# Optimization experiments

Hardware: AMD Instinct MI355X
Metric: run time of the kernel (lower is better)

## Reference

```python
import jax, jax.numpy as jnp
import numpy as np

VOCAB = 50000
SEQ = 2048
BATCH = 64
D = 256


def setup_inputs() -> dict:
    key = jax.random.key(0)
    ks = jax.random.split(key, 9)
    x = jax.random.randint(ks[0], (SEQ, BATCH), 0, VOCAB)  # token ids, 0 = pad
    emb = jax.random.normal(ks[1], (VOCAB, D), jnp.float32) * 0.02
    emb = emb.at[0].set(0.0)  # padding_idx=0
    idf = jax.random.uniform(ks[2], (VOCAB,), jnp.float32, 0.1, 10.0)
    W1 = jax.random.normal(ks[3], (100, D), jnp.float32) * (1.0 / np.sqrt(D))
    b1 = jax.random.normal(ks[4], (100,), jnp.float32) * 0.01
    W2 = jax.random.normal(ks[5], (150, 100), jnp.float32) * 0.1
    b2 = jax.random.normal(ks[6], (150,), jnp.float32) * 0.01
    W3 = jax.random.normal(ks[7], (2, 150), jnp.float32) * 0.1
    b3 = jax.random.normal(ks[8], (2,), jnp.float32) * 0.01
    return {"x": x, "emb": emb, "idf": idf, "W1": W1, "b1": b1,
            "W2": W2, "b2": b2, "W3": W3, "b3": b3}


def reference(x, emb, idf, W1, b1, W2, b2, W3, b3):
    tokens = x.T  # [B, S] (nums = x.permute(1, 0))
    vocab = emb.shape[0]

    # per-row term frequency: histogram (scatter-add) then gather back
    def tf_row(row):  # row: [S] int
        return jnp.zeros((vocab,), jnp.float32).at[row].add(1.0)[row]

    tf = jax.vmap(tf_row)(tokens)                      # [B, S]
    scores = jnp.where(tokens == 0, 0.0, tf * idf[tokens])  # [B, S]

    # bmm of (B, D, S) with (B, S, 1) == tf-idf weighted sum of embeddings
    pooled = jnp.einsum('bsd,bs->bd', emb[tokens], scores)  # [B, D]

    h = jax.nn.relu(pooled @ W1.T + b1)
    h = jax.nn.relu(h @ W2.T + b2)
    return jax.nn.softmax(h @ W3.T + b3, axis=-1)  # [B, 2]
```

## Files before the change

kernel.cpp:

```cpp
#include <hip/hip_runtime.h>

#define VOCAB 50000
#define SEQ   2048
#define BATCH 64
#define DIM   256
#define NC    16
#define CHUNK (SEQ / NC)
#define H1    100
#define H2    150
#define HASH  4096

__global__ __launch_bounds__(1024)
void k_scores(const int* __restrict__ x,
              const float* __restrict__ idf,
              float* __restrict__ scores) {
    __shared__ int   tok[SEQ];
    __shared__ int   hkey[HASH];
    __shared__ int   hcnt[HASH];
    const int b = blockIdx.x;
    const int t = threadIdx.x;

    for (int i = t; i < HASH; i += 1024) { hkey[i] = -1; hcnt[i] = 0; }
    for (int s = t; s < SEQ; s += 1024)  tok[s] = x[s * BATCH + b];
    __syncthreads();

    for (int s = t; s < SEQ; s += 1024) {
        const int mytok = tok[s];
        unsigned h = ((unsigned)mytok * 2654435761u) >> 20;
        while (true) {
            int prev = atomicCAS(&hkey[h], -1, mytok);
            if (prev == -1 || prev == mytok) { atomicAdd(&hcnt[h], 1); break; }
            h = (h + 1) & (HASH - 1);
        }
    }
    __syncthreads();

    for (int s = t; s < SEQ; s += 1024) {
        const int mytok = tok[s];
        unsigned h = ((unsigned)mytok * 2654435761u) >> 20;
        while (hkey[h] != mytok) h = (h + 1) & (HASH - 1);
        float sc = (mytok == 0) ? 0.0f : (float)hcnt[h] * idf[mytok];
        scores[b * SEQ + s] = sc;
    }
}

__global__ __launch_bounds__(256)
void k_pool(const int* __restrict__ x,
            const float* __restrict__ emb,
            const float* __restrict__ scores,
            float* __restrict__ partials) {
    __shared__ int   tok[CHUNK];
    __shared__ float sc[CHUNK];
    __shared__ float acc_lds[4][DIM];
    const int c = blockIdx.x;
    const int b = blockIdx.y;
    const int t = threadIdx.x;
    const int wave = t >> 6, lane = t & 63;
    const int s0 = c * CHUNK;

    if (t < CHUNK) {
        tok[t] = x[(s0 + t) * BATCH + b];
        sc[t]  = scores[b * SEQ + s0 + t];
    }
    __syncthreads();

    float4 acc = make_float4(0.f, 0.f, 0.f, 0.f);
    for (int i = wave; i < CHUNK; i += 4) {
        const float s = sc[i];
        const float4 v = ((const float4*)(emb + (size_t)tok[i] * DIM))[lane];
        acc.x = fmaf(v.x, s, acc.x);
        acc.y = fmaf(v.y, s, acc.y);
        acc.z = fmaf(v.z, s, acc.z);
        acc.w = fmaf(v.w, s, acc.w);
    }
    ((float4*)acc_lds[wave])[lane] = acc;
    __syncthreads();

    if (t < DIM) {
        float r = acc_lds[0][t] + acc_lds[1][t] + acc_lds[2][t] + acc_lds[3][t];
        partials[((size_t)c * BATCH + b) * DIM + t] = r;
    }
}

__global__ __launch_bounds__(256)
void k_mlp(const float* __restrict__ partials,
           const float* __restrict__ W1, const float* __restrict__ b1,
           const float* __restrict__ W2, const float* __restrict__ b2,
           const float* __restrict__ W3, const float* __restrict__ b3,
           float* __restrict__ out) {
    __shared__ float pld[DIM];
    __shared__ float h1[112];
    __shared__ float h2[152];
    __shared__ float logit[2];
    const int b = blockIdx.x;
    const int t = threadIdx.x;
    const int wave = t >> 6, lane = t & 63;

    float a = 0.0f;
#pragma unroll
    for (int c = 0; c < NC; ++c)
        a += partials[((size_t)c * BATCH + b) * DIM + t];
    pld[t] = a;
    __syncthreads();

    for (int j = wave; j < H1; j += 4) {
        const float4 wv = ((const float4*)(W1 + j * DIM))[lane];
        const float4 pv = ((const float4*)pld)[lane];
        float d = wv.x * pv.x + wv.y * pv.y + wv.z * pv.z + wv.w * pv.w;
#pragma unroll
        for (int off = 32; off; off >>= 1) d += __shfl_down(d, off);
        if (lane == 0) h1[j] = fmaxf(d + b1[j], 0.0f);
    }
    __syncthreads();

    for (int j = wave; j < H2; j += 4) {
        float d = 0.0f;
        if (lane < 25) {
            const float4 wv = ((const float4*)(W2 + j * H1))[lane];
            const float4 hv = ((const float4*)h1)[lane];
            d = wv.x * hv.x + wv.y * hv.y + wv.z * hv.z + wv.w * hv.w;
        }
#pragma unroll
        for (int off = 32; off; off >>= 1) d += __shfl_down(d, off);
        if (lane == 0) h2[j] = fmaxf(d + b2[j], 0.0f);
    }
    __syncthreads();

    if (wave < 2) {
        const int j = wave;
        float d = 0.0f;
        for (int k = lane; k < H2; k += 64) d += W3[j * H2 + k] * h2[k];
#pragma unroll
        for (int off = 32; off; off >>= 1) d += __shfl_down(d, off);
        if (lane == 0) logit[j] = d + b3[j];
    }
    __syncthreads();

    if (t == 0) {
        const float m  = fmaxf(logit[0], logit[1]);
        const float e0 = __expf(logit[0] - m);
        const float e1 = __expf(logit[1] - m);
        const float inv = 1.0f / (e0 + e1);
        out[b * 2 + 0] = e0 * inv;
        out[b * 2 + 1] = e1 * inv;
    }
}

extern "C" void kernel_launch(void* const* d_in, const int* in_sizes, int n_in,
                              void* d_out, int out_size, void* d_ws, size_t ws_size,
                              hipStream_t stream) {
    const int*   x   = (const int*)  d_in[0];
    const float* emb = (const float*)d_in[1];
    const float* idf = (const float*)d_in[2];
    const float* W1  = (const float*)d_in[3];
    const float* b1  = (const float*)d_in[4];
    const float* W2  = (const float*)d_in[5];
    const float* b2  = (const float*)d_in[6];
    const float* W3  = (const float*)d_in[7];
    const float* b3  = (const float*)d_in[8];
    float* out = (float*)d_out;

    float* scores   = (float*)d_ws;
    float* partials = scores + (size_t)BATCH * SEQ;

    k_scores<<<BATCH, 1024, 0, stream>>>(x, idf, scores);
    k_pool  <<<dim3(NC, BATCH), 256, 0, stream>>>(x, emb, scores, partials);
    k_mlp   <<<BATCH, 256, 0, stream>>>(partials, W1, b1, W2, b2, W3, b3, out);
}
```

Baseline: 158.4 us.

## Restructure MLP as batched GEMM kernels with weights broadcast across batch lanes

The per-sample MLP kernel (one block per batch row, re-reading weights 64 times) is replaced by two kernels. The first transposes the pooled vectors into LDS and has each lane own one batch element, computing layer 1 with wave-uniform weight loads across 4 blocks. The second runs layers 2 and 3 plus softmax for all 64 samples in a single block. This cuts redundant weight traffic and the cross-lane reductions, but adds a kernel launch and leaves layers 2-3 serialized on one workgroup with very low parallelism.

```diff
diff --git a/kernel.cpp b/kernel.cpp
--- a/kernel.cpp
+++ b/kernel.cpp
@@ -82,67 +82,100 @@
     }
 }
 
-__global__ __launch_bounds__(256)
-void k_mlp(const float* __restrict__ partials,
-           const float* __restrict__ W1, const float* __restrict__ b1,
-           const float* __restrict__ W2, const float* __restrict__ b2,
-           const float* __restrict__ W3, const float* __restrict__ b3,
-           float* __restrict__ out) {
-    __shared__ float pld[DIM];
-    __shared__ float h1[112];
-    __shared__ float h2[152];
-    __shared__ float logit[2];
-    const int b = blockIdx.x;
-    const int t = threadIdx.x;
-    const int wave = t >> 6, lane = t & 63;
-
-    float a = 0.0f;
-#pragma unroll
-    for (int c = 0; c < NC; ++c)
-        a += partials[((size_t)c * BATCH + b) * DIM + t];
-    pld[t] = a;
-    __syncthreads();
-
-    for (int j = wave; j < H1; j += 4) {
-        const float4 wv = ((const float4*)(W1 + j * DIM))[lane];
-        const float4 pv = ((const float4*)pld)[lane];
-        float d = wv.x * pv.x + wv.y * pv.y + wv.z * pv.z + wv.w * pv.w;
-#pragma unroll
-        for (int off = 32; off; off >>= 1) d += __shfl_down(d, off);
-        if (lane == 0) h1[j] = fmaxf(d + b1[j], 0.0f);
-    }
-    __syncthreads();
-
-    for (int j = wave; j < H2; j += 4) {
-        float d = 0.0f;
-        if (lane < 25) {
-            const float4 wv = ((const float4*)(W2 + j * H1))[lane];
-            const float4 hv = ((const float4*)h1)[lane];
-            d = wv.x * hv.x + wv.y * hv.y + wv.z * hv.z + wv.w * hv.w;
-        }
-#pragma unroll
-        for (int off = 32; off; off >>= 1) d += __shfl_down(d, off);
-        if (lane == 0) h2[j] = fmaxf(d + b2[j], 0.0f);
-    }
-    __syncthreads();
-
-    if (wave < 2) {
-        const int j = wave;
-        float d = 0.0f;
-        for (int k = lane; k < H2; k += 64) d += W3[j * H2 + k] * h2[k];
-#pragma unroll
-        for (int off = 32; off; off >>= 1) d += __shfl_down(d, off);
-        if (lane == 0) logit[j] = d + b3[j];
-    }
-    __syncthreads();
-
-    if (t == 0) {
-        const float m  = fmaxf(logit[0], logit[1]);
-        const float e0 = __expf(logit[0] - m);
-        const float e1 = __expf(logit[1] - m);
+#define PT_LD 65
+__global__ __launch_bounds__(1024)
+void k_mlp1(const float* __restrict__ partials,
+            const float* __restrict__ W1, const float* __restrict__ b1,
+            float* __restrict__ h1T) {
+    __shared__ float pooledT[DIM * PT_LD];
+    const int t = threadIdx.x;
+    const int w = t >> 6, lane = t & 63;
+    const int base = 25 * blockIdx.x;
+
+#pragma unroll
+    for (int n = 0; n < 16; ++n) {
+        const int i = n * 1024 + t;
+        const int b = i >> 8, d = i & 255;
+        float a = 0.0f;
+#pragma unroll
+        for (int c = 0; c < NC; ++c)
+            a += partials[c * (BATCH * DIM) + i];
+        pooledT[d * PT_LD + b] = a;
+    }
+    __syncthreads();
+
+    {
+        const int j0 = __builtin_amdgcn_readfirstlane(base + w);
+        const bool has1 = (16 + w) < 25;
+        const int j1 = __builtin_amdgcn_readfirstlane(base + ((16 + w) < 25 ? 16 + w : 0));
+        float a0 = 0.0f, a1 = 0.0f;
+#pragma unroll 8
+        for (int k = 0; k < DIM; ++k) {
+            const float v = pooledT[k * PT_LD + lane];
+            a0 = fmaf(v, W1[j0 * DIM + k], a0);
+            a1 = fmaf(v, W1[j1 * DIM + k], a1);
+        }
+        h1T[j0 * BATCH + lane] = fmaxf(a0 + b1[j0], 0.0f);
+        if (has1) h1T[j1 * BATCH + lane] = fmaxf(a1 + b1[j1], 0.0f);
+    }
+}
+
+__global__ __launch_bounds__(1024)
+void k_mlp2(const float* __restrict__ h1T,
+            const float* __restrict__ W2, const float* __restrict__ b2,
+            const float* __restrict__ W3, const float* __restrict__ b3,
+            float* __restrict__ out) {
+    __shared__ float h1s[H1 * BATCH];
+    __shared__ float h2s[H2 * BATCH];
+    __shared__ float lg[2][BATCH];
+    const int t = threadIdx.x;
+    const int w = t >> 6, lane = t & 63;
+
+    for (int i = t; i < H1 * BATCH; i += 1024) h1s[i] = h1T[i];
+    __syncthreads();
+
+    {
+        float acc[10];
+        int   jj[10];
+        bool  valid[10];
+#pragma unroll
+        for (int i = 0; i < 10; ++i) {
+            const int j = w + 16 * i;
+            valid[i] = (j < H2);
+            jj[i] = __builtin_amdgcn_readfirstlane(valid[i] ? j : 0);
+            acc[i] = 0.0f;
+        }
+#pragma unroll 4
+        for (int k = 0; k < H1; ++k) {
+            const float v = h1s[k * BATCH + lane];
+#pragma unroll
+            for (int i = 0; i < 10; ++i)
+                acc[i] = fmaf(v, W2[jj[i] * H1 + k], acc[i]);
+        }
+#pragma unroll
+        for (int i = 0; i < 10; ++i)
+            if (valid[i]) h2s[jj[i] * BATCH + lane] = fmaxf(acc[i] + b2[jj[i]], 0.0f);
+    }
+    __syncthreads();
+
+    if (w < 2) {
+        const int j = __builtin_amdgcn_readfirstlane(w);
+        float a = 0.0f;
+#pragma unroll 5
+        for (int k = 0; k < H2; ++k)
+            a = fmaf(h2s[k * BATCH + lane], W3[j * H2 + k], a);
+        lg[j][lane] = a + b3[j];
+    }
+    __syncthreads();
+
+    if (t < BATCH) {
+        const float l0 = lg[0][t], l1 = lg[1][t];
+        const float m  = fmaxf(l0, l1);
+        const float e0 = __expf(l0 - m);
+        const float e1 = __expf(l1 - m);
         const float inv = 1.0f / (e0 + e1);
-        out[b * 2 + 0] = e0 * inv;
-        out[b * 2 + 1] = e1 * inv;
+        out[t * 2 + 0] = e0 * inv;
+        out[t * 2 + 1] = e1 * inv;
     }
 }
 
@@ -162,8 +195,10 @@
 
     float* scores   = (float*)d_ws;
     float* partials = scores + (size_t)BATCH * SEQ;
+    float* h1T      = partials + (size_t)NC * BATCH * DIM;
 
     k_scores<<<BATCH, 1024, 0, stream>>>(x, idf, scores);
     k_pool  <<<dim3(NC, BATCH), 256, 0, stream>>>(x, emb, scores, partials);
-    k_mlp   <<<BATCH, 256, 0, stream>>>(partials, W1, b1, W2, b2, W3, b3, out);
-}
+    k_mlp1  <<<4, 1024, 0, stream>>>(partials, W1, b1, h1T);
+    k_mlp2  <<<1, 1024, 0, stream>>>(h1T, W2, b2, W3, b3, out);
+}
```

Result: slower. 169.0 us (+6.7%).

## Fuse scoring, pooling and MLP into a single per-batch kernel

Applied to the files above, without the earlier changes.

Merges the tf-idf scoring, embedding pooling and MLP head into one kernel with one 1024-thread block per batch row, keeping scores and pooled vectors in shared memory. This removes two kernel launches and the global round-trips for scores and partial sums. The MLP layers are also re-split across threads as four-way partial dot products. In exchange, the gather-heavy pooling stage now runs on only 64 blocks instead of 1024, which limits how many compute units pull embedding rows.

```diff
diff --git a/kernel.cpp b/kernel.cpp
--- a/kernel.cpp
+++ b/kernel.cpp
@@ -4,27 +4,46 @@
 #define SEQ   2048
 #define BATCH 64
 #define DIM   256
-#define NC    16
-#define CHUNK (SEQ / NC)
 #define H1    100
 #define H2    150
 #define HASH  4096
+#define NW    16
 
 __global__ __launch_bounds__(1024)
-void k_scores(const int* __restrict__ x,
-              const float* __restrict__ idf,
-              float* __restrict__ scores) {
+void k_fused(const int* __restrict__ x,
+             const float* __restrict__ emb,
+             const float* __restrict__ idf,
+             const float* __restrict__ W1, const float* __restrict__ b1,
+             const float* __restrict__ W2, const float* __restrict__ b2,
+             const float* __restrict__ W3, const float* __restrict__ b3,
+             float* __restrict__ out) {
     __shared__ int   tok[SEQ];
     __shared__ int   hkey[HASH];
     __shared__ int   hcnt[HASH];
+    __shared__ float sc[SEQ];
+    __shared__ float wacc[NW][DIM];
+    __shared__ float pooled[DIM];
+    __shared__ float hp1[128][4];
+    __shared__ float h1s[H1];
+    __shared__ float hp2[H2][4];
+    __shared__ float h2s[H2];
+    __shared__ float lg[2];
+
     const int b = blockIdx.x;
     const int t = threadIdx.x;
+    const int w = t >> 6, lane = t & 63;
 
     for (int i = t; i < HASH; i += 1024) { hkey[i] = -1; hcnt[i] = 0; }
-    for (int s = t; s < SEQ; s += 1024)  tok[s] = x[s * BATCH + b];
+#pragma unroll
+    for (int n = 0; n < SEQ / 1024; ++n) {
+        const int s = n * 1024 + t;
+        tok[s] = x[s * BATCH + b];
+    }
     __syncthreads();
 
-    for (int s = t; s < SEQ; s += 1024) {
+#pragma unroll
+    for (int n = 0; n < SEQ / 1024; ++n) {
+        const int s = n * 1024 + t;
         const int mytok = tok[s];
         unsigned h = ((unsigned)mytok * 2654435761u) >> 20;
         while (true) {
@@ -35,111 +54,89 @@
     }
     __syncthreads();
 
-    for (int s = t; s < SEQ; s += 1024) {
+#pragma unroll
+    for (int n = 0; n < SEQ / 1024; ++n) {
+        const int s = n * 1024 + t;
         const int mytok = tok[s];
         unsigned h = ((unsigned)mytok * 2654435761u) >> 20;
         while (hkey[h] != mytok) h = (h + 1) & (HASH - 1);
-        float sc = (mytok == 0) ? 0.0f : (float)hcnt[h] * idf[mytok];
-        scores[b * SEQ + s] = sc;
-    }
-}
-
-__global__ __launch_bounds__(256)
-void k_pool(const int* __restrict__ x,
-            const float* __restrict__ emb,
-            const float* __restrict__ scores,
-            float* __restrict__ partials) {
-    __shared__ int   tok[CHUNK];
-    __shared__ float sc[CHUNK];
-    __shared__ float acc_lds[4][DIM];
-    const int c = blockIdx.x;
-    const int b = blockIdx.y;
-    const int t = threadIdx.x;
-    const int wave = t >> 6, lane = t & 63;
-    const int s0 = c * CHUNK;
-
-    if (t < CHUNK) {
-        tok[t] = x[(s0 + t) * BATCH + b];
-        sc[t]  = scores[b * SEQ + s0 + t];
+        sc[s] = (mytok == 0) ? 0.0f : (float)hcnt[h] * idf[mytok];
     }
     __syncthreads();
 
-    float4 acc = make_float4(0.f, 0.f, 0.f, 0.f);
-    for (int i = wave; i < CHUNK; i += 4) {
-        const float s = sc[i];
-        const float4 v = ((const float4*)(emb + (size_t)tok[i] * DIM))[lane];
-        acc.x = fmaf(v.x, s, acc.x);
-        acc.y = fmaf(v.y, s, acc.y);
-        acc.z = fmaf(v.z, s, acc.z);
-        acc.w = fmaf(v.w, s, acc.w);
+    {
+        const float4* embv = (const float4*)emb;
+        float4 acc = make_float4(0.f, 0.f, 0.f, 0.f);
+        const int s0 = w * (SEQ / NW);
+#pragma unroll 4
+        for (int i = 0; i < SEQ / NW; ++i) {
+            const int s = s0 + i;
+            const float sv = sc[s];
+            const float4 v = embv[(size_t)tok[s] * (DIM / 4) + lane];
+            acc.x = fmaf(v.x, sv, acc.x);
+            acc.y = fmaf(v.y, sv, acc.y);
+            acc.z = fmaf(v.z, sv, acc.z);
+            acc.w = fmaf(v.w, sv, acc.w);
+        }
+        ((float4*)wacc[w])[lane] = acc;
     }
-    ((float4*)acc_lds[wave])[lane] = acc;
     __syncthreads();
 
     if (t < DIM) {
-        float r = acc_lds[0][t] + acc_lds[1][t] + acc_lds[2][t] + acc_lds[3][t];
-        partials[((size_t)c * BATCH + b) * DIM + t] = r;
-    }
-}
-
-__global__ __launch_bounds__(256)
-void k_mlp(const float* __restrict__ partials,
-           const float* __restrict__ W1, const float* __restrict__ b1,
-           const float* __restrict__ W2, const float* __restrict__ b2,
-           const float* __restrict__ W3, const float* __restrict__ b3,
-           float* __restrict__ out) {
-    __shared__ float pld[DIM];
-    __shared__ float h1[112];
-    __shared__ float h2[152];
-    __shared__ float logit[2];
-    const int b = blockIdx.x;
-    const int t = threadIdx.x;
-    const int wave = t >> 6, lane = t & 63;
-
-    float a = 0.0f;
+        float a = 0.0f;
 #pragma unroll
-    for (int c = 0; c < NC; ++c)
-        a += partials[((size_t)c * BATCH + b) * DIM + t];
-    pld[t] = a;
-    __syncthreads();
-
-    for (int j = wave; j < H1; j += 4) {
-        const float4 wv = ((const float4*)(W1 + j * DIM))[lane];
-        const float4 pv = ((const float4*)pld)[lane];
-        float d = wv.x * pv.x + wv.y * pv.y + wv.z * pv.z + wv.w * pv.w;
-#pragma unroll
-        for (int off = 32; off; off >>= 1) d += __shfl_down(d, off);
-        if (lane == 0) h1[j] = fmaxf(d + b1[j], 0.0f);
+        for (int i = 0; i < NW; ++i) a += wacc[i][t];
+        pooled[t] = a;
     }
     __syncthreads();
 
-    for (int j = wave; j < H2; j += 4) {
-        float d = 0.0f;
-        if (lane < 25) {
-            const float4 wv = ((const float4*)(W2 + j * H1))[lane];
-            const float4 hv = ((const float4*)h1)[lane];
-            d = wv.x * hv.x + wv.y * hv.y + wv.z * hv.z + wv.w * hv.w;
+    if (t < 512) {
+        const int j = t >> 2;
+        const int q = t & 3;
+        if (j < H1) {
+            const float4* wv = (const float4*)(W1 + j * DIM + q * 64);
+            const float4* pv = (const float4*)(pooled) + q * 16;
+            float a = 0.0f;
+#pragma unroll
+            for (int i = 0; i < 16; ++i) {
+                const float4 ww = wv[i];
+                const float4 pp = pv[i];
+                a += ww.x * pp.x + ww.y * pp.y + ww.z * pp.z + ww.w * pp.w;
+            }
+            hp1[j][q] = a;
         }
-#pragma unroll
-        for (int off = 32; off; off >>= 1) d += __shfl_down(d, off);
-        if (lane == 0) h2[j] = fmaxf(d + b2[j], 0.0f);
     }
     __syncthreads();
+    if (t < H1)
+        h1s[t] = fmaxf(hp1[t][0] + hp1[t][1] + hp1[t][2] + hp1[t][3] + b1[t], 0.0f);
+    __syncthreads();
 
-    if (wave < 2) {
-        const int j = wave;
-        float d = 0.0f;
-        for (int k = lane; k < H2; k += 64) d += W3[j * H2 + k] * h2[k];
+    if (t < 600) {
+        const int j = t >> 2;
+        const int q = t & 3;
+        const float* wv = W2 + j * H1 + q * 25;
+        float a = 0.0f;
 #pragma unroll
-        for (int off = 32; off; off >>= 1) d += __shfl_down(d, off);
-        if (lane == 0) logit[j] = d + b3[j];
+        for (int i = 0; i < 25; ++i)
+            a = fmaf(wv[i], h1s[q * 25 + i], a);
+        hp2[j][q] = a;
     }
     __syncthreads();
+    if (t < H2)
+        h2s[t] = fmaxf(hp2[t][0] + hp2[t][1] + hp2[t][2] + hp2[t][3] + b2[t], 0.0f);
+    __syncthreads();
 
+    if (t < 2) {
+        const float* wv = W3 + t * H2;
+        float a = b3[t];
+        for (int k = 0; k < H2; ++k) a = fmaf(wv[k], h2s[k], a);
+        lg[t] = a;
+    }
+    __syncthreads();
     if (t == 0) {
-        const float m  = fmaxf(logit[0], logit[1]);
-        const float e0 = __expf(logit[0] - m);
-        const float e1 = __expf(logit[1] - m);
+        const float m  = fmaxf(lg[0], lg[1]);
+        const float e0 = __expf(lg[0] - m);
+        const float e1 = __expf(lg[1] - m);
         const float inv = 1.0f / (e0 + e1);
         out[b * 2 + 0] = e0 * inv;
         out[b * 2 + 1] = e1 * inv;
@@ -160,10 +157,5 @@
     const float* b3  = (const float*)d_in[8];
     float* out = (float*)d_out;
 
-    float* scores   = (float*)d_ws;
-    float* partials = scores + (size_t)BATCH * SEQ;
-
-    k_scores<<<BATCH, 1024, 0, stream>>>(x, idf, scores);
-    k_pool  <<<dim3(NC, BATCH), 256, 0, stream>>>(x, emb, scores, partials);
-    k_mlp   <<<BATCH, 256, 0, stream>>>(partials, W1, b1, W2, b2, W3, b3, out);
+    k_fused<<<BATCH, 1024, 0, stream>>>(x, emb, idf, W1, b1, W2, b2, W3, b3, out);
 }
```

Result: faster. 129.4 us (-18.3%).
